# Optimization experiments

Measured on AMD Instinct MI355X. Metric: run time of the kernel, lower is better.

## Reference

```python
import jax, jax.numpy as jnp
import numpy as np

PC_MIN = jnp.array([0.0, -40.0, -3.0], dtype=jnp.float32)
VS_TOP = jnp.array([0.4, 0.4, 4.0], dtype=jnp.float32)
VS_MED = jnp.array([0.2, 0.2, 2.0], dtype=jnp.float32)
VS_LOW = jnp.array([0.1, 0.1, 1.0], dtype=jnp.float32)
GRID_TOP = (176, 200, 1)
GRID_MED = (352, 400, 2)
GRID_LOW = (704, 800, 4)
EPS = 1e-3
FILL = np.iinfo(np.int32).max


def _bn(x, g, b):
    # training-mode BatchNorm1d over the point/voxel axis (naiveSyncBN1d, eps=1e-3)
    mu = jnp.mean(x, axis=0)
    var = jnp.var(x, axis=0)
    return (x - mu) * jax.lax.rsqrt(var + EPS) * g + b


def _decode(lin, gx, gy, gz):
    x = lin % gx
    r = lin // gx
    y = r % gy
    r = r // gy
    z = r % gz
    b = r // gz
    return b, x, y, z


def _vfe(pts, batch, vs, grid, W1, g1, b1, W2, g2, b2):
    # Dynamic voxelization + DynamicScatterVFE (cluster center + voxel center, 2 layers, scatter-mean).
    N = pts.shape[0]
    gx, gy, gz = grid
    xyz = pts[:, :3]
    coors = jnp.floor((xyz - PC_MIN) / vs).astype(jnp.int32)
    cx = jnp.clip(coors[:, 0], 0, gx - 1)
    cy = jnp.clip(coors[:, 1], 0, gy - 1)
    cz = jnp.clip(coors[:, 2], 0, gz - 1)
    lin = ((batch * gz + cz) * gy + cy) * gx + cx  # linear voxel id incl. batch
    uniq, inv = jnp.unique(lin, return_inverse=True, size=N, fill_value=FILL)
    valid = uniq != FILL
    cnt = jnp.maximum(jax.ops.segment_sum(jnp.ones((N,), pts.dtype), inv, num_segments=N), 1.0)
    seg_mean = lambda v: jax.ops.segment_sum(v, inv, num_segments=N) / cnt[:, None]
    f_cluster = xyz - seg_mean(xyz)[inv]                      # offset from per-voxel point mean
    centers = PC_MIN + (jnp.stack([cx, cy, cz], axis=1).astype(pts.dtype) + 0.5) * vs
    f_center = xyz - centers                                   # offset from voxel center
    feats = jnp.concatenate([pts, f_cluster, f_center], axis=1)  # [N, 10]
    h = jax.nn.relu(_bn(feats @ W1, g1, b1))
    h = jnp.concatenate([h, seg_mean(h)[inv]], axis=1)           # point feat || gathered voxel feat
    h = jax.nn.relu(_bn(h @ W2, g2, b2))
    vox = seg_mean(h)
    return jnp.where(valid[:, None], vox, 0.0), uniq, valid


def _merge(sub_feats, sub_uniq, sub_valid, top_uniq, sub_grid, factor):
    # find_coordinate_indices + scatter_v2(mode='avg'): mean of child voxel feats per parent voxel.
    b, x, y, z = _decode(sub_uniq, *sub_grid)
    gx, gy, gz = GRID_TOP
    parent = ((b * gz + z // factor) * gy + y // factor) * gx + x // factor
    M = top_uniq.shape[0]
    pos = jnp.clip(jnp.searchsorted(top_uniq, parent), 0, M - 1)
    found = sub_valid & (top_uniq[pos] == parent)
    seg = jnp.where(found, pos, M)  # unmatched/padding rows dropped into slot M
    s = jax.ops.segment_sum(sub_feats, seg, num_segments=M + 1)[:M]
    c = jax.ops.segment_sum(found.astype(sub_feats.dtype), seg, num_segments=M + 1)[:M]
    return s / jnp.maximum(c, 1.0)[:, None]


def setup_inputs() -> dict:
    key = jax.random.key(0)
    ks = jax.random.split(key, 12)
    N, B = 262144, 2
    x = jax.random.uniform(ks[0], (N, 1), jnp.float32, 0.0, 70.4)
    y = jax.random.uniform(ks[1], (N, 1), jnp.float32, -40.0, 40.0)
    z = jax.random.uniform(ks[2], (N, 1), jnp.float32, -3.0, 1.0)
    inten = jax.random.uniform(ks[3], (N, 1), jnp.float32)
    bcol = jnp.repeat(jnp.arange(B, dtype=jnp.float32), N // B)[:, None]
    points = jnp.concatenate([bcol, x, y, z, inten], axis=1)
    lin_w = lambda k, i, o: jax.random.normal(k, (i, o), jnp.float32) * (1.0 / np.sqrt(i))
    return dict(
        points=points, batch_size=2,
        W1_top=lin_w(ks[4], 10, 64), g1_top=jnp.ones(64), b1_top=jnp.zeros(64),
        W2_top=lin_w(ks[5], 128, 128), g2_top=jnp.ones(128), b2_top=jnp.zeros(128),
        W1_med=lin_w(ks[6], 10, 32), g1_med=jnp.ones(32), b1_med=jnp.zeros(32),
        W2_med=lin_w(ks[7], 64, 64), g2_med=jnp.ones(64), b2_med=jnp.zeros(64),
        W1_low=lin_w(ks[8], 10, 32), g1_low=jnp.ones(32), b1_low=jnp.zeros(32),
        W2_low=lin_w(ks[9], 64, 64), g2_low=jnp.ones(64), b2_low=jnp.zeros(64),
    )


def reference(points, batch_size, W1_top, g1_top, b1_top, W2_top, g2_top, b2_top,
              W1_med, g1_med, b1_med, W2_med, g2_med, b2_med,
              W1_low, g1_low, b1_low, W2_low, g2_low, b2_low):
    batch = points[:, 0].astype(jnp.int32)
    pts = points[:, 1:]
    vf, top_uniq, top_valid = _vfe(pts, batch, VS_TOP, GRID_TOP, W1_top, g1_top, b1_top, W2_top, g2_top, b2_top)
    mfeat, med_uniq, med_valid = _vfe(pts, batch, VS_MED, GRID_MED, W1_med, g1_med, b1_med, W2_med, g2_med, b2_med)
    lfeat, low_uniq, low_valid = _vfe(pts, batch, VS_LOW, GRID_LOW, W1_low, g1_low, b1_low, W2_low, g2_low, b2_low)
    med_mean = _merge(mfeat, med_uniq, med_valid, top_uniq, GRID_MED, 2)
    low_mean = _merge(lfeat, low_uniq, low_valid, top_uniq, GRID_LOW, 4)
    merged = jnp.where(top_valid[:, None], jnp.concatenate([med_mean, low_mean], axis=1), 0.0)
    b, x, y, z = _decode(top_uniq, *GRID_TOP)
    coors = jnp.where(top_valid[:, None], jnp.stack([b, z, y, x], axis=1), -1)
    return vf, merged, coors
```

## Files before the change

### kernel.cpp

```cpp
#include <hip/hip_runtime.h>
#include <cstdint>
#include <cstddef>

#define NPTS 262144
#define BLK 256
#define TGX 176
#define TGY 200
#define TGZ 1

#define G_TOPC 70400
#define G_MEDC 1126400
#define G_LOWC 4505600

#define SCAN_ITEMS 32
#define SCAN_CHUNK (BLK*SCAN_ITEMS)
#define NB_T 9
#define NB_M 138
#define NB_L 550
#define BO_T 0
#define BO_M 16
#define BO_L 160
#define NBVT (G_TOPC/BLK)
#define NBVM (NPTS/BLK)
#define NBVL (NPTS/BLK)

#define Y2B2 (NPTS/64)
#define ST1BLKS 256
#define NHT 4400
#define NHM 8192
#define NJT 8800
#define NJM 16384
#define NCL 275

typedef __attribute__((ext_vector_type(8))) short bf16x8;
typedef __attribute__((ext_vector_type(4))) float f32x4;

struct SP {
  const float4* srt; const int* jr; const float4* vm;
  const float* W1; const float* W2;
  const float* g1; const float* b1; const float* g2; const float* b2;
  const int* cnt; const int* uniq; const int* woff; const int* U;
  float* segt; float* part1; float* part2;
  float* coef1; float* coef2;
  unsigned short* Y2;
  float* hout;
  int C1; int segstride; int gx, gy, gz; float vx, vy, vz;
};

__device__ __forceinline__ unsigned short f2bf(float v) {
  unsigned u = __float_as_uint(v);
  u += 0x7FFFu + ((u >> 16) & 1u);
  return (unsigned short)(u >> 16);
}
__device__ __forceinline__ float bf2f(unsigned short h) {
  return __uint_as_float((unsigned)h << 16);
}

__device__ __forceinline__ void pcoords(float x, float y, float z,
    float vx, float vy, float vz, int gx, int gy, int gz,
    int& cx, int& cy, int& cz) {
  cx = (int)floorf((x - 0.0f)  / vx);
  cy = (int)floorf((y + 40.0f) / vy);
  cz = (int)floorf((z + 3.0f)  / vz);
  cx = min(max(cx, 0), gx - 1);
  cy = min(max(cy, 0), gy - 1);
  cz = min(max(cz, 0), gz - 1);
}

__device__ __forceinline__ int lin3(float b, float x, float y, float z,
    float vx, float vy, float vz, int gx, int gy, int gz) {
  int cx, cy, cz; pcoords(x, y, z, vx, vy, vz, gx, gy, gz, cx, cy, cz);
  return (((int)b * gz + cz) * gy + cy) * gx + cx;
}

__device__ __forceinline__ void build_f(float4 p, float4 vm,
    float vx, float vy, float vz, int gx, int gy, int gz, float* f) {
  int cx, cy, cz; pcoords(p.x, p.y, p.z, vx, vy, vz, gx, gy, gz, cx, cy, cz);
  f[0] = p.x; f[1] = p.y; f[2] = p.z; f[3] = p.w;
  f[4] = p.x - vm.x;
  f[5] = p.y - vm.y;
  f[6] = p.z - vm.z;
  f[7] = p.x - (0.0f   + (cx + 0.5f)*vx);
  f[8] = p.y - (-40.0f + (cy + 0.5f)*vy);
  f[9] = p.z - (-3.0f  + (cz + 0.5f)*vz);
}

__global__ __launch_bounds__(BLK) void k_count3(const float* __restrict__ pts,
    int* __restrict__ ct, int* __restrict__ cm, int* __restrict__ cl) {
  int i = blockIdx.x * BLK + threadIdx.x;
  if (i >= NPTS) return;
  float b = pts[i*5+0], x = pts[i*5+1], y = pts[i*5+2], z = pts[i*5+3];
  atomicAdd(&ct[lin3(b,x,y,z, 0.4f,0.4f,4.0f, 176,200,1)], 1);
  atomicAdd(&cm[lin3(b,x,y,z, 0.2f,0.2f,2.0f, 352,400,2)], 1);
  atomicAdd(&cl[lin3(b,x,y,z, 0.1f,0.1f,1.0f, 704,800,4)], 1);
}

__global__ __launch_bounds__(BLK) void k_scan1_all(const int* __restrict__ ct,
    const int* __restrict__ cm, const int* __restrict__ cl,
    int2* __restrict__ bsum) {
  int bid = blockIdx.x;
  const int* cnt; int G, bo, cb;
  if (bid < NB_T)            { cnt = ct; G = G_TOPC; bo = BO_T; cb = bid; }
  else if (bid < NB_T+NB_M)  { cnt = cm; G = G_MEDC; bo = BO_M; cb = bid - NB_T; }
  else                       { cnt = cl; G = G_LOWC; bo = BO_L; cb = bid - NB_T - NB_M; }
  int base = cb * SCAN_CHUNK + threadIdx.x * SCAN_ITEMS;
  int so = 0, sp = 0;
  #pragma unroll
  for (int k = 0; k < SCAN_ITEMS; k++) {
    int j = base + k;
    if (j < G) { int c = cnt[j]; if (c > 0) { so++; sp += c; } }
  }
  __shared__ int sho[BLK], shp[BLK];
  sho[threadIdx.x] = so; shp[threadIdx.x] = sp; __syncthreads();
  for (int off = BLK/2; off > 0; off >>= 1) {
    if (threadIdx.x < off) {
      sho[threadIdx.x] += sho[threadIdx.x + off];
      shp[threadIdx.x] += shp[threadIdx.x + off];
    }
    __syncthreads();
  }
  if (threadIdx.x == 0) { int2 v; v.x = sho[0]; v.y = shp[0]; bsum[bo + cb] = v; }
}

__device__ void scan_pass(int2* bsum, int off, int nb, int* U,
                          int* so, int* sp) {
  int t = threadIdx.x;
  int vo = 0, vp = 0;
  if (t < nb) { int2 v = bsum[off + t]; vo = v.x; vp = v.y; }
  so[t] = vo; sp[t] = vp; __syncthreads();
  for (int o = 1; o < 1024; o <<= 1) {
    int ao = (t >= o) ? so[t - o] : 0;
    int ap = (t >= o) ? sp[t - o] : 0;
    __syncthreads();
    so[t] += ao; sp[t] += ap;
    __syncthreads();
  }
  if (t < nb) { int2 e; e.x = so[t] - vo; e.y = sp[t] - vp; bsum[off + t] = e; }
  if (t == 0) *U = so[1023];
  __syncthreads();
}

__global__ __launch_bounds__(1024) void k_scan2_all(int2* __restrict__ bsum,
    int* __restrict__ Ut, int* __restrict__ Um, int* __restrict__ Ul) {
  __shared__ int so[1024], sp[1024];
  scan_pass(bsum, BO_T, NB_T, Ut, so, sp);
  scan_pass(bsum, BO_M, NB_M, Um, so, sp);
  scan_pass(bsum, BO_L, NB_L, Ul, so, sp);
}

__global__ __launch_bounds__(BLK) void k_scan3_all(const int* __restrict__ ct,
    const int* __restrict__ cm, const int* __restrict__ cl,
    const int2* __restrict__ bsum,
    int* __restrict__ rkt, int* __restrict__ rkm, int* __restrict__ rkl,
    int* __restrict__ uqt, int* __restrict__ uqm, int* __restrict__ uql,
    int* __restrict__ wot, int* __restrict__ wom, int* __restrict__ wol) {
  int bid = blockIdx.x;
  const int* cnt; int G, bo, cb; int *rank, *uniq, *woff;
  if (bid < NB_T)           { cnt=ct; G=G_TOPC; bo=BO_T; cb=bid;            rank=rkt; uniq=uqt; woff=wot; }
  else if (bid < NB_T+NB_M) { cnt=cm; G=G_MEDC; bo=BO_M; cb=bid-NB_T;       rank=rkm; uniq=uqm; woff=wom; }
  else                      { cnt=cl; G=G_LOWC; bo=BO_L; cb=bid-NB_T-NB_M;  rank=rkl; uniq=uql; woff=wol; }
  int base = cb * SCAN_CHUNK + threadIdx.x * SCAN_ITEMS;
  int so = 0, sp = 0;
  #pragma unroll
  for (int k = 0; k < SCAN_ITEMS; k++) {
    int j = base + k;
    if (j < G) { int c = cnt[j]; if (c > 0) { so++; sp += c; } }
  }
  __shared__ int sho[BLK], shp[BLK];
  sho[threadIdx.x] = so; shp[threadIdx.x] = sp; __syncthreads();
  for (int off = 1; off < BLK; off <<= 1) {
    int ao = (threadIdx.x >= off) ? sho[threadIdx.x - off] : 0;
    int ap = (threadIdx.x >= off) ? shp[threadIdx.x - off] : 0;
    __syncthreads();
    sho[threadIdx.x] += ao; shp[threadIdx.x] += ap;
    __syncthreads();
  }
  int2 bb = bsum[bo + cb];
  int ro = bb.x + sho[threadIdx.x] - so;
  int po = bb.y + shp[threadIdx.x] - sp;
  for (int k = 0; k < SCAN_ITEMS; k++) {
    int j = base + k;
    if (j < G) {
      int c = cnt[j];
      if (c > 0) { rank[j] = ro; uniq[ro] = j; woff[ro] = po; ro++; po += c; }
    }
  }
}

__global__ __launch_bounds__(BLK) void k_scatter3(const float* __restrict__ pts,
    const int* __restrict__ rkt, int* __restrict__ wot, float4* __restrict__ st, int* __restrict__ jt,
    const int* __restrict__ rkm, int* __restrict__ wom, float4* __restrict__ sm, int* __restrict__ jm,
    const int* __restrict__ rkl, int* __restrict__ wol, float4* __restrict__ sl, int* __restrict__ jl) {
  int i = blockIdx.x * BLK + threadIdx.x;
  if (i >= NPTS) return;
  float b = pts[i*5+0], x = pts[i*5+1], y = pts[i*5+2], z = pts[i*5+3], it = pts[i*5+4];
  float4 p; p.x = x; p.y = y; p.z = z; p.w = it;
  {
    int r = rkt[lin3(b,x,y,z, 0.4f,0.4f,4.0f, 176,200,1)];
    int j = atomicAdd(&wot[r], 1); st[j] = p; jt[j] = r;
  }
  {
    int r = rkm[lin3(b,x,y,z, 0.2f,0.2f,2.0f, 352,400,2)];
    int j = atomicAdd(&wom[r], 1); sm[j] = p; jm[j] = r;
  }
  {
    int r = rkl[lin3(b,x,y,z, 0.1f,0.1f,1.0f, 704,800,4)];
    int j = atomicAdd(&wol[r], 1); sl[j] = p; jl[j] = r;
  }
}

__global__ __launch_bounds__(BLK) void k_vox13(
    const float4* __restrict__ st, const int* __restrict__ uqt, const int* __restrict__ ct,
    const int* __restrict__ wot, const int* __restrict__ Ut, float4* __restrict__ vt,
    const float4* __restrict__ sm, const int* __restrict__ uqm, const int* __restrict__ cm,
    const int* __restrict__ wom, const int* __restrict__ Um, float4* __restrict__ vm,
    const float4* __restrict__ sl, const int* __restrict__ uql, const int* __restrict__ cl,
    const int* __restrict__ wol, const int* __restrict__ Ul, float4* __restrict__ vl) {
  int bid = blockIdx.x;
  const float4* srt; const int *uniq, *cnt, *woff, *Up; float4* vmean; int r;
  if (bid < NBVT)           { r = bid*BLK + threadIdx.x;           srt=st; uniq=uqt; cnt=ct; woff=wot; Up=Ut; vmean=vt; }
  else if (bid < NBVT+NBVM) { r = (bid-NBVT)*BLK + threadIdx.x;    srt=sm; uniq=uqm; cnt=cm; woff=wom; Up=Um; vmean=vm; }
  else                      { r = (bid-NBVT-NBVM)*BLK + threadIdx.x; srt=sl; uniq=uql; cnt=cl; woff=wol; Up=Ul; vmean=vl; }
  if (r >= *Up) return;
  int lin = uniq[r];
  int len = cnt[lin];
  int base = woff[r] - len;
  float sx = 0.f, sy = 0.f, sz = 0.f;
  for (int k = 0; k < len; k++) {
    float4 p = srt[base + k];
    sx += p.x; sy += p.y; sz += p.z;
  }
  float il = 1.0f / (float)len;
  float4 o; o.x = sx*il; o.y = sy*il; o.z = sz*il; o.w = il;
  vmean[r] = o;
}

__global__ __launch_bounds__(BLK) void k_stats1_all(SP a, SP b, SP c) {
  int s = blockIdx.x >> 8;
  int blk = blockIdx.x & 255;
  SP sp = (s == 0) ? a : ((s == 1) ? b : c);
  const int C1 = sp.C1;
  __shared__ float w[640];
  __shared__ float wsum[4][64], wsq[4][64];
  for (int t = threadIdx.x; t < 10*C1; t += BLK) w[t] = sp.W1[t];
  __syncthreads();
  float f[4][10];
  #pragma unroll
  for (int k = 0; k < 4; k++) {
    int i = blk*1024 + k*BLK + threadIdx.x;
    float4 p = sp.srt[i];
    float4 vmn = sp.vm[sp.jr[i]];
    build_f(p, vmn, sp.vx, sp.vy, sp.vz, sp.gx, sp.gy, sp.gz, f[k]);
  }
  int wv = threadIdx.x >> 6;
  int lane = threadIdx.x & 63;
  for (int o = 0; o < C1; o += 4) {
    float sacc[4] = {0,0,0,0}, qacc[4] = {0,0,0,0};
    #pragma unroll
    for (int k = 0; k < 4; k++) {
      float a0=0.f, a1=0.f, a2=0.f, a3=0.f;
      #pragma unroll
      for (int d = 0; d < 10; d++) {
        float fv = f[k][d];
        const float* wr = &w[d*C1 + o];
        a0 = fmaf(fv, wr[0], a0); a1 = fmaf(fv, wr[1], a1);
        a2 = fmaf(fv, wr[2], a2); a3 = fmaf(fv, wr[3], a3);
      }
      sacc[0] += a0; sacc[1] += a1; sacc[2] += a2; sacc[3] += a3;
      qacc[0] += a0*a0; qacc[1] += a1*a1; qacc[2] += a2*a2; qacc[3] += a3*a3;
    }
    #pragma unroll
    for (int m = 1; m < 64; m <<= 1) {
      #pragma unroll
      for (int e = 0; e < 4; e++) {
        sacc[e] += __shfl_xor(sacc[e], m);
        qacc[e] += __shfl_xor(qacc[e], m);
      }
    }
    if (lane == 0) {
      #pragma unroll
      for (int e = 0; e < 4; e++) { wsum[wv][o+e] = sacc[e]; wsq[wv][o+e] = qacc[e]; }
    }
  }
  __syncthreads();
  if (threadIdx.x < C1) {
    int ch = threadIdx.x;
    float sv = wsum[0][ch] + wsum[1][ch] + wsum[2][ch] + wsum[3][ch];
    float qv = wsq[0][ch] + wsq[1][ch] + wsq[2][ch] + wsq[3][ch];
    sp.part1[(size_t)blk*2*C1 + ch]      = sv;
    sp.part1[(size_t)blk*2*C1 + C1 + ch] = qv;
  }
}

__device__ __forceinline__ void partcoef_body(const float* part, int NB, int C,
    int ch, const float* g, const float* b, float* coef) {
  float s = 0.f, q = 0.f;
  for (int bk = threadIdx.x; bk < NB; bk += BLK) {
    s += part[(size_t)bk*2*C + ch];
    q += part[(size_t)bk*2*C + C + ch];
  }
  __shared__ float ss[BLK], sq[BLK];
  ss[threadIdx.x] = s; sq[threadIdx.x] = q; __syncthreads();
  for (int off = BLK/2; off > 0; off >>= 1) {
    if (threadIdx.x < off) {
      ss[threadIdx.x] += ss[threadIdx.x + off];
      sq[threadIdx.x] += sq[threadIdx.x + off];
    }
    __syncthreads();
  }
  if (threadIdx.x == 0) {
    float mu  = ss[0] * (1.0f / NPTS);
    float var = sq[0] * (1.0f / NPTS) - mu*mu;
    float sc  = g[ch] * (1.0f / sqrtf(var + 1e-3f));
    coef[ch]     = sc;
    coef[C + ch] = fmaf(-mu, sc, b[ch]);
  }
}

__global__ __launch_bounds__(BLK) void k_partcoef1_all(SP a, SP b, SP c) {
  int bid = blockIdx.x; SP sp; int ch;
  if (bid < 64)      { sp = a; ch = bid; }
  else if (bid < 96) { sp = b; ch = bid - 64; }
  else               { sp = c; ch = bid - 96; }
  if (ch >= sp.C1) return;
  partcoef_body(sp.part1, ST1BLKS, sp.C1, ch, sp.g1, sp.b1, sp.coef1);
}

__global__ __launch_bounds__(BLK) void k_partcoef2_all(SP a, SP b, SP c) {
  int bid = blockIdx.x; SP sp; int ch;
  if (bid < 128)      { sp = a; ch = bid; }
  else if (bid < 192) { sp = b; ch = bid - 128; }
  else                { sp = c; ch = bid - 192; }
  if (ch >= 2*sp.C1) return;
  partcoef_body(sp.part2, Y2B2, 2*sp.C1, ch, sp.g2, sp.b2, sp.coef2);
}

__global__ __launch_bounds__(BLK) void k_hsegT_all(SP a, SP b, SP c) {
  int bid = blockIdx.x; SP sp; int rb;
  if (bid < NHT)           { sp = a; rb = bid; }
  else if (bid < NHT+NHM)  { sp = b; rb = bid - NHT; }
  else                     { sp = c; rb = bid - NHT - NHM; }
  const int C1 = sp.C1;
  const int qsh = (C1 == 64) ? 4 : 3;
  __shared__ float w[640];
  __shared__ float sc[64], sb[64];
  for (int t = threadIdx.x; t < 10*C1; t += BLK) w[t] = sp.W1[t];
  for (int t = threadIdx.x; t < C1; t += BLK) { sc[t] = sp.coef1[t]; sb[t] = sp.coef1[C1 + t]; }
  __syncthreads();
  int tid = rb * BLK + threadIdx.x;
  int r = tid >> qsh;
  int q = tid & ((1 << qsh) - 1);
  if (r >= *sp.U) return;
  int lin = sp.uniq[r];
  int len = sp.cnt[lin];
  int base = sp.woff[r] - len;
  float4 vmn = sp.vm[r];
  int c0 = q * 4;
  float s0 = sc[c0+0], s1 = sc[c0+1], s2 = sc[c0+2], s3 = sc[c0+3];
  float o0 = sb[c0+0], o1 = sb[c0+1], o2 = sb[c0+2], o3 = sb[c0+3];
  float a0=0.f, a1=0.f, a2=0.f, a3=0.f;
  for (int k = 0; k < len; k++) {
    float4 p = sp.srt[base + k];
    float f[10];
    build_f(p, vmn, sp.vx, sp.vy, sp.vz, sp.gx, sp.gy, sp.gz, f);
    float y0=0.f, y1=0.f, y2=0.f, y3=0.f;
    #pragma unroll
    for (int d = 0; d < 10; d++) {
      float fv = f[d];
      const float* wr = &w[d*C1 + c0];
      y0 = fmaf(fv, wr[0], y0); y1 = fmaf(fv, wr[1], y1);
      y2 = fmaf(fv, wr[2], y2); y3 = fmaf(fv, wr[3], y3);
    }
    a0 += fmaxf(fmaf(y0, s0, o0), 0.f);
    a1 += fmaxf(fmaf(y1, s1, o1), 0.f);
    a2 += fmaxf(fmaf(y2, s2, o2), 0.f);
    a3 += fmaxf(fmaf(y3, s3, o3), 0.f);
  }
  float il = 1.0f / (float)len;
  sp.segt[(size_t)(c0+0)*sp.segstride + r] = a0*il;
  sp.segt[(size_t)(c0+1)*sp.segstride + r] = a1*il;
  sp.segt[(size_t)(c0+2)*sp.segstride + r] = a2*il;
  sp.segt[(size_t)(c0+3)*sp.segstride + r] = a3*il;
}

__global__ __launch_bounds__(BLK) void k_packB_all(
    const float* __restrict__ W2t_, unsigned short* __restrict__ Bt,
    const float* __restrict__ W2m_, unsigned short* __restrict__ Bm,
    const float* __restrict__ W2l_, unsigned short* __restrict__ Bl) {
  int bid = blockIdx.x;
  const float* W2; unsigned short* Bp; int C2, idx;
  if (bid < 64)      { W2 = W2t_; Bp = Bt; C2 = 128; idx = bid*BLK + threadIdx.x; }
  else if (bid < 80) { W2 = W2m_; Bp = Bm; C2 = 64;  idx = (bid-64)*BLK + threadIdx.x; }
  else               { W2 = W2l_; Bp = Bl; C2 = 64;  idx = (bid-80)*BLK + threadIdx.x; }
  if (idx >= C2*C2) return;
  int NCF = C2/16;
  int per_kb = NCF*512;
  int kb = idx / per_kb, rem = idx % per_kb;
  int cf = rem / 512, r2 = rem % 512;
  int lane = r2 >> 3, j = r2 & 7;
  int k = kb*32 + (lane >> 4)*8 + j;
  int col = cf*16 + (lane & 15);
  Bp[idx] = f2bf(W2[(size_t)k*C2 + col]);
}

template<int C1>
__device__ __forceinline__ void y2m_body(const SP& sp,
    const unsigned short* __restrict__ Bpk, int blk, unsigned short* Alds) {
  constexpr int K   = 2*C1;
  constexpr int C2  = 2*C1;
  constexpr int MT  = 64;
  constexpr int NKB = K / 32;
  constexpr int NCF = C2 / 16;
  constexpr int RB  = K * 2;
  const int tid  = threadIdx.x;
  const int base = blk * MT;

  {
    const int jst = tid & 63;
    const int qst = tid >> 6;
    int jr = sp.jr[base + jst];
    float4 p = sp.srt[base + jst];
    float4 vmn = sp.vm[jr];
    float fs[10];
    build_f(p, vmn, sp.vx, sp.vy, sp.vz, sp.gx, sp.gy, sp.gz, fs);
    const int k_lo = qst * (K/4);
    #pragma unroll
    for (int kk = 0; kk < K/8; kk++) {
      int k0 = k_lo + kk*2;
      float v0, v1;
      if (k0 < C1) {
        float y0 = 0.f, y1v = 0.f;
        #pragma unroll
        for (int d = 0; d < 10; d++) {
          y0  = fmaf(fs[d], sp.W1[d*C1 + k0],     y0);
          y1v = fmaf(fs[d], sp.W1[d*C1 + k0 + 1], y1v);
        }
        v0 = fmaxf(fmaf(y0,  sp.coef1[k0],   sp.coef1[C1 + k0]),   0.f);
        v1 = fmaxf(fmaf(y1v, sp.coef1[k0+1], sp.coef1[C1 + k0+1]), 0.f);
      } else {
        v0 = sp.segt[(size_t)(k0     - C1)*sp.segstride + jr];
        v1 = sp.segt[(size_t)(k0 + 1 - C1)*sp.segstride + jr];
      }
      unsigned u = (unsigned)f2bf(v0) | ((unsigned)f2bf(v1) << 16);
      int g  = k0 >> 3;
      int gp = g ^ (jst & 7);
      *(unsigned*)((char*)Alds + (size_t)jst*RB + gp*16 + (k0 & 7)*2) = u;
    }
  }
  __syncthreads();

  const int w    = tid >> 6;
  const int l    = tid & 63;
  const int rowf = l & 15;
  const int kg   = l >> 4;
  const int row  = w*16 + rowf;
  f32x4 acc[NCF];
  #pragma unroll
  for (int cf = 0; cf < NCF; cf++) acc[cf] = (f32x4){0.f, 0.f, 0.f, 0.f};
  #pragma unroll
  for (int kb = 0; kb < NKB; kb++) {
    int g  = kb*4 + kg;
    int gp = g ^ (row & 7);
    bf16x8 a = *(const bf16x8*)((const char*)Alds + (size_t)row*RB + gp*16);
    const bf16x8* bfr = (const bf16x8*)Bpk + (size_t)(kb*NCF)*64 + l;
    #pragma unroll
    for (int cf = 0; cf < NCF; cf++) {
      bf16x8 b = bfr[cf*64];
      acc[cf] = __builtin_amdgcn_mfma_f32_16x16x32_bf16(a, b, acc[cf], 0, 0, 0);
    }
  }

  __syncthreads();
  float* red = (float*)Alds;
  #pragma unroll
  for (int cf = 0; cf < NCF; cf++) {
    f32x4 v = acc[cf];
    float sv = v.x + v.y + v.z + v.w;
    float qv = v.x*v.x + v.y*v.y + v.z*v.z + v.w*v.w;
    red[(w*4 + kg)*C2 + cf*16 + rowf]        = sv;
    red[(16 + w*4 + kg)*C2 + cf*16 + rowf]   = qv;
  }
  __syncthreads();
  if (tid < C2) {
    float sv = 0.f, qv = 0.f;
    #pragma unroll 4
    for (int i = 0; i < 16; i++) {
      sv += red[i*C2 + tid];
      qv += red[(16 + i)*C2 + tid];
    }
    sp.part2[(size_t)blk*2*C2 + tid]      = sv;
    sp.part2[(size_t)blk*2*C2 + C2 + tid] = qv;
  }
  __syncthreads();

  unsigned short* D = Alds;
  #pragma unroll
  for (int cf = 0; cf < NCF; cf++) {
    #pragma unroll
    for (int rg = 0; rg < 4; rg++) {
      int rr = w*16 + kg*4 + rg;
      D[rr*C2 + cf*16 + rowf] = f2bf(acc[cf][rg]);
    }
  }
  __syncthreads();
  for (int it = tid; it < MT*C2/8; it += BLK) {
    int r = (it*8) / C2;
    int c = (it*8) % C2;
    uint4 v = *(const uint4*)&D[it*8];
    *(uint4*)&sp.Y2[(size_t)(base + r)*C2 + c] = v;
  }
}

__global__ __launch_bounds__(BLK) void k_y2m_all(SP a, SP b, SP c,
    const unsigned short* __restrict__ Bt, const unsigned short* __restrict__ Bm,
    const unsigned short* __restrict__ Bl) {
  __shared__ unsigned short Alds[64*128];
  int bid = blockIdx.x;
  if (bid < Y2B2)        y2m_body<64>(a, Bt, bid, Alds);
  else if (bid < 2*Y2B2) y2m_body<32>(b, Bm, bid - Y2B2, Alds);
  else                   y2m_body<32>(c, Bl, bid - 2*Y2B2, Alds);
}

__global__ __launch_bounds__(BLK) void k_hseg2_all(SP a, SP b, SP c) {
  int bid = blockIdx.x; SP sp; int rb;
  if (bid < NJT)           { sp = a; rb = bid; }
  else if (bid < NJT+NJM)  { sp = b; rb = bid - NJT; }
  else                     { sp = c; rb = bid - NJT - NJM; }
  const int C = 2*sp.C1;
  const int qsh = (C == 128) ? 5 : 4;
  __shared__ float sc[128], sb[128];
  for (int t = threadIdx.x; t < C; t += BLK) { sc[t] = sp.coef2[t]; sb[t] = sp.coef2[C + t]; }
  __syncthreads();
  int tid = rb * BLK + threadIdx.x;
  int r = tid >> qsh;
  int q = tid & ((1 << qsh) - 1);
  if (r >= *sp.U) return;
  int lin = sp.uniq[r];
  int len = sp.cnt[lin];
  int base = sp.woff[r] - len;
  int c0 = q * 4;
  float s0 = sc[c0+0], s1 = sc[c0+1], s2 = sc[c0+2], s3 = sc[c0+3];
  float o0 = sb[c0+0], o1 = sb[c0+1], o2 = sb[c0+2], o3 = sb[c0+3];
  float a0=0.f, a1=0.f, a2=0.f, a3=0.f;
  const unsigned short* Yh = sp.Y2;
  for (int k = 0; k < len; k++) {
    ushort4 hv = *(const ushort4*)&Yh[(size_t)(base + k)*C + c0];
    a0 += fmaxf(fmaf(bf2f(hv.x), s0, o0), 0.f);
    a1 += fmaxf(fmaf(bf2f(hv.y), s1, o1), 0.f);
    a2 += fmaxf(fmaf(bf2f(hv.z), s2, o2), 0.f);
    a3 += fmaxf(fmaf(bf2f(hv.w), s3, o3), 0.f);
  }
  float il = 1.0f / (float)len;
  float4 o = {a0*il, a1*il, a2*il, a3*il};
  *(float4*)&sp.hout[(size_t)r*C + c0] = o;
}

__global__ __launch_bounds__(BLK) void k_clist_all(const int* __restrict__ tuniq,
    const int* __restrict__ Utp,
    const int* __restrict__ cnt_m, const int* __restrict__ rank_m,
    int* __restrict__ clist_m, int* __restrict__ mcnt_m,
    const int* __restrict__ cnt_l, const int* __restrict__ rank_l,
    int* __restrict__ clist_l, int* __restrict__ mcnt_l) {
  int bid = blockIdx.x;
  const int *scnt, *srank; int *clist, *mcnt;
  int gx, gy, gz, f, rb;
  if (bid < NCL) { scnt=cnt_m; srank=rank_m; clist=clist_m; mcnt=mcnt_m;
                   gx=352; gy=400; gz=2; f=2; rb=bid; }
  else           { scnt=cnt_l; srank=rank_l; clist=clist_l; mcnt=mcnt_l;
                   gx=704; gy=800; gz=4; f=4; rb=bid-NCL; }
  int r = rb * BLK + threadIdx.x;
  if (r >= *Utp) return;
  int lin = tuniq[r];
  int x = lin % TGX; int t = lin / TGX;
  int y = t % TGY;   int b = t / TGY;
  int m = 0;
  for (int cz = 0; cz < gz; cz++)
    for (int yy = y*f; yy < y*f + f; yy++)
      for (int xx = x*f; xx < x*f + f; xx++) {
        int cl = ((b*gz + cz)*gy + yy)*gx + xx;
        if (scnt[cl] > 0) clist[(size_t)r*64 + (m++)] = srank[cl];
      }
  mcnt[r] = m;
}

__global__ __launch_bounds__(BLK) void k_merge2_all(
    const float* __restrict__ vox_m, const int* __restrict__ clist_m,
    const int* __restrict__ mcnt_m, float* __restrict__ maccm,
    const float* __restrict__ vox_l, const int* __restrict__ clist_l,
    const int* __restrict__ mcnt_l, float* __restrict__ maccl,
    const int* __restrict__ Utp) {
  int bid = blockIdx.x;
  const float* vox; const int *clist, *mcnt; float* dest; int rb;
  if (bid < NHT) { vox=vox_m; clist=clist_m; mcnt=mcnt_m; dest=maccm; rb=bid; }
  else           { vox=vox_l; clist=clist_l; mcnt=mcnt_l; dest=maccl; rb=bid-NHT; }
  int idx = rb * BLK + threadIdx.x;
  int r = idx >> 4;
  int q = idx & 15;
  if (r >= *Utp) return;
  int m = mcnt[r];
  float a0=0.f, a1=0.f, a2=0.f, a3=0.f;
  for (int t = 0; t < m; t++) {
    int cr = clist[(size_t)r*64 + t];
    float4 v = *(const float4*)&vox[(size_t)cr*64 + q*4];
    a0 += v.x; a1 += v.y; a2 += v.z; a3 += v.w;
  }
  float inv = 1.0f / (float)max(m, 1);
  float4 o = {a0*inv, a1*inv, a2*inv, a3*inv};
  *(float4*)&dest[(size_t)r*64 + q*4] = o;
}

__global__ __launch_bounds__(BLK) void k_fin_all(const int* __restrict__ uniq,
    const int* __restrict__ Up, const float* __restrict__ maccm,
    const float* __restrict__ maccl, float* __restrict__ vf,
    float* __restrict__ mg, float* __restrict__ coors) {
  int idx = blockIdx.x * BLK + threadIdx.x;
  int r = idx >> 5;
  int q = idx & 31;
  if (r >= NPTS) return;
  int U = *Up;
  float4 v = {0.f, 0.f, 0.f, 0.f};
  if (r < U)
    v = (q < 16) ? *(const float4*)&maccm[(size_t)r*64 + q*4]
                 : *(const float4*)&maccl[(size_t)r*64 + (q-16)*4];
  *(float4*)&mg[(size_t)r*128 + q*4] = v;
  if (r >= U) {
    float4 z = {0.f, 0.f, 0.f, 0.f};
    *(float4*)&vf[(size_t)r*128 + q*4] = z;
  }
  if (q == 0) {
    float4 co;
    if (r < U) {
      int lin = uniq[r];
      int x = lin % TGX; int t = lin / TGX;
      int y = t % TGY;   t /= TGY;
      int z = t % TGZ;   int b = t / TGZ;
      co.x = (float)b; co.y = (float)z; co.z = (float)y; co.w = (float)x;
    } else {
      co.x = -1.f; co.y = -1.f; co.z = -1.f; co.w = -1.f;
    }
    *(float4*)&coors[(size_t)r*4] = co;
  }
}

extern "C" void kernel_launch(void* const* d_in, const int* in_sizes, int n_in,
                              void* d_out, int out_size, void* d_ws, size_t ws_size,
                              hipStream_t stream) {
  const float* pts = (const float*)d_in[0];

  float* out = (float*)d_out;
  float* vf = out;
  float* mg = out + (size_t)NPTS * 128;
  float* co = out + (size_t)NPTS * 256;

  char* w = (char*)d_ws;
  size_t off = 0;
  auto alloc = [&](size_t bytes) -> void* {
    void* p = w + off;
    off = (off + bytes + 1023) & ~(size_t)1023;
    return p;
  };
  int*    cnt_t   = (int*)alloc(((size_t)G_TOPC + G_MEDC + G_LOWC) * 4);
  int*    cnt_m   = cnt_t + G_TOPC;
  int*    cnt_l   = cnt_t + G_TOPC + G_MEDC;
  int*    rank_t  = (int*)alloc((size_t)G_TOPC * 4);
  int*    rank_m  = (int*)alloc((size_t)G_MEDC * 4);
  int*    rank_l  = (int*)alloc((size_t)G_LOWC * 4);
  int*    uniq_t  = (int*)alloc((size_t)G_TOPC * 4);
  int*    uniq_m  = (int*)alloc((size_t)NPTS * 4);
  int*    uniq_l  = (int*)alloc((size_t)NPTS * 4);
  int*    woff_t  = (int*)alloc((size_t)G_TOPC * 4);
  int*    woff_m  = (int*)alloc((size_t)NPTS * 4);
  int*    woff_l  = (int*)alloc((size_t)NPTS * 4);
  float4* srt_t   = (float4*)alloc((size_t)NPTS * 16);
  float4* srt_m   = (float4*)alloc((size_t)NPTS * 16);
  float4* srt_l   = (float4*)alloc((size_t)NPTS * 16);
  int*    jr_t    = (int*)alloc((size_t)NPTS * 4);
  int*    jr_m    = (int*)alloc((size_t)NPTS * 4);
  int*    jr_l    = (int*)alloc((size_t)NPTS * 4);
  float4* vm_t    = (float4*)alloc((size_t)G_TOPC * 16);
  float4* vm_m    = (float4*)alloc((size_t)NPTS * 16);
  float4* vm_l    = (float4*)alloc((size_t)NPTS * 16);
  float*  segt_t  = (float*)alloc((size_t)G_TOPC * 64 * 4);
  float*  segt_m  = (float*)alloc((size_t)NPTS * 32 * 4);
  float*  segt_l  = (float*)alloc((size_t)NPTS * 32 * 4);
  float*  vox_m   = (float*)alloc((size_t)NPTS * 64 * 4);
  float*  vox_l   = (float*)alloc((size_t)NPTS * 64 * 4);
  unsigned short* Y2h_t = (unsigned short*)alloc((size_t)NPTS * 128 * 2);
  unsigned short* Y2h_m = (unsigned short*)alloc((size_t)NPTS * 64 * 2);
  unsigned short* Y2h_l = (unsigned short*)alloc((size_t)NPTS * 64 * 2);
  unsigned short* Bpk_t = (unsigned short*)alloc(16384 * 2);
  unsigned short* Bpk_m = (unsigned short*)alloc(4096 * 2);
  unsigned short* Bpk_l = (unsigned short*)alloc(4096 * 2);
  int*    clist_m = (int*)alloc((size_t)G_TOPC * 64 * 4);
  int*    clist_l = (int*)alloc((size_t)G_TOPC * 64 * 4);
  int*    mcnt_m  = (int*)alloc((size_t)G_TOPC * 4);
  int*    mcnt_l  = (int*)alloc((size_t)G_TOPC * 4);
  float*  maccm   = (float*)alloc((size_t)G_TOPC * 64 * 4);
  float*  maccl   = (float*)alloc((size_t)G_TOPC * 64 * 4);
  float*  part1_t = (float*)alloc((size_t)ST1BLKS * 128 * 4);
  float*  part1_m = (float*)alloc((size_t)ST1BLKS * 64 * 4);
  float*  part1_l = (float*)alloc((size_t)ST1BLKS * 64 * 4);
  float*  part2_t = (float*)alloc((size_t)Y2B2 * 256 * 4);
  float*  part2_m = (float*)alloc((size_t)Y2B2 * 128 * 4);
  float*  part2_l = (float*)alloc((size_t)Y2B2 * 128 * 4);
  float*  coef    = (float*)alloc(6 * 256 * 4);
  int2*   bsum    = (int2*)alloc(1024 * 8);
  int*    Ut      = (int*)alloc(64);
  int*    Um      = (int*)alloc(64);
  int*    Ul      = (int*)alloc(64);
  (void)in_sizes; (void)n_in; (void)out_size; (void)ws_size;

  auto mkSP = [&](int scaleIdx) -> SP {
    SP s{};
    if (scaleIdx == 0) {
      s.srt = srt_t; s.jr = jr_t; s.vm = vm_t;
      s.W1 = (const float*)d_in[2];  s.g1 = (const float*)d_in[3];
      s.b1 = (const float*)d_in[4];  s.W2 = (const float*)d_in[5];
      s.g2 = (const float*)d_in[6];  s.b2 = (const float*)d_in[7];
      s.cnt = cnt_t; s.uniq = uniq_t; s.woff = woff_t; s.U = Ut;
      s.segt = segt_t; s.part1 = part1_t; s.part2 = part2_t;
      s.coef1 = coef + 0*256; s.coef2 = coef + 1*256;
      s.Y2 = Y2h_t; s.hout = vf;
      s.C1 = 64; s.segstride = G_TOPC;
      s.gx = 176; s.gy = 200; s.gz = 1; s.vx = 0.4f; s.vy = 0.4f; s.vz = 4.0f;
    } else if (scaleIdx == 1) {
      s.srt = srt_m; s.jr = jr_m; s.vm = vm_m;
      s.W1 = (const float*)d_in[8];  s.g1 = (const float*)d_in[9];
      s.b1 = (const float*)d_in[10]; s.W2 = (const float*)d_in[11];
      s.g2 = (const float*)d_in[12]; s.b2 = (const float*)d_in[13];
      s.cnt = cnt_m; s.uniq = uniq_m; s.woff = woff_m; s.U = Um;
      s.segt = segt_m; s.part1 = part1_m; s.part2 = part2_m;
      s.coef1 = coef + 2*256; s.coef2 = coef + 3*256;
      s.Y2 = Y2h_m; s.hout = vox_m;
      s.C1 = 32; s.segstride = NPTS;
      s.gx = 352; s.gy = 400; s.gz = 2; s.vx = 0.2f; s.vy = 0.2f; s.vz = 2.0f;
    } else {
      s.srt = srt_l; s.jr = jr_l; s.vm = vm_l;
      s.W1 = (const float*)d_in[14]; s.g1 = (const float*)d_in[15];
      s.b1 = (const float*)d_in[16]; s.W2 = (const float*)d_in[17];
      s.g2 = (const float*)d_in[18]; s.b2 = (const float*)d_in[19];
      s.cnt = cnt_l; s.uniq = uniq_l; s.woff = woff_l; s.U = Ul;
      s.segt = segt_l; s.part1 = part1_l; s.part2 = part2_l;
      s.coef1 = coef + 4*256; s.coef2 = coef + 5*256;
      s.Y2 = Y2h_l; s.hout = vox_l;
      s.C1 = 32; s.segstride = NPTS;
      s.gx = 704; s.gy = 800; s.gz = 4; s.vx = 0.1f; s.vy = 0.1f; s.vz = 1.0f;
    }
    return s;
  };
  SP spT = mkSP(0), spM = mkSP(1), spL = mkSP(2);

  k_packB_all<<<96, BLK, 0, stream>>>((const float*)d_in[5], Bpk_t,
      (const float*)d_in[11], Bpk_m, (const float*)d_in[17], Bpk_l);

  (void)hipMemsetAsync(cnt_t, 0, ((size_t)G_TOPC + G_MEDC + G_LOWC) * 4, stream);
  k_count3<<<NPTS/BLK, BLK, 0, stream>>>(pts, cnt_t, cnt_m, cnt_l);
  k_scan1_all<<<NB_T + NB_M + NB_L, BLK, 0, stream>>>(cnt_t, cnt_m, cnt_l, bsum);
  k_scan2_all<<<1, 1024, 0, stream>>>(bsum, Ut, Um, Ul);
  k_scan3_all<<<NB_T + NB_M + NB_L, BLK, 0, stream>>>(cnt_t, cnt_m, cnt_l, bsum,
      rank_t, rank_m, rank_l, uniq_t, uniq_m, uniq_l, woff_t, woff_m, woff_l);
  k_clist_all<<<2*NCL, BLK, 0, stream>>>(uniq_t, Ut,
      cnt_m, rank_m, clist_m, mcnt_m, cnt_l, rank_l, clist_l, mcnt_l);
  k_scatter3<<<NPTS/BLK, BLK, 0, stream>>>(pts,
      rank_t, woff_t, srt_t, jr_t,
      rank_m, woff_m, srt_m, jr_m,
      rank_l, woff_l, srt_l, jr_l);
  k_vox13<<<NBVT + NBVM + NBVL, BLK, 0, stream>>>(
      srt_t, uniq_t, cnt_t, woff_t, Ut, vm_t,
      srt_m, uniq_m, cnt_m, woff_m, Um, vm_m,
      srt_l, uniq_l, cnt_l, woff_l, Ul, vm_l);

  k_stats1_all<<<3*ST1BLKS, BLK, 0, stream>>>(spT, spM, spL);
  k_partcoef1_all<<<128, BLK, 0, stream>>>(spT, spM, spL);
  k_hsegT_all<<<NHT + 2*NHM, BLK, 0, stream>>>(spT, spM, spL);
  k_y2m_all<<<3*Y2B2, BLK, 0, stream>>>(spT, spM, spL, Bpk_t, Bpk_m, Bpk_l);
  k_partcoef2_all<<<256, BLK, 0, stream>>>(spT, spM, spL);
  k_hseg2_all<<<NJT + 2*NJM, BLK, 0, stream>>>(spT, spM, spL);

  k_merge2_all<<<2*NHT, BLK, 0, stream>>>(vox_m, clist_m, mcnt_m, maccm,
      vox_l, clist_l, mcnt_l, maccl, Ut);
  k_fin_all<<<(NPTS*32)/BLK, BLK, 0, stream>>>(uniq_t, Ut, maccm, maccl,
      vf, mg, co);
}
```

Baseline: 692.1 us.

## Compute BN1 stats from feature moments and write merge output directly into final buffer

The first BatchNorm's mean and variance are now derived from the first and second moments of the 10-dim input features (10 sums plus 55 cross-products) instead of computing all C1 projected channels per point. A tiny 3-block kernel reduces the moments and projects them through W1 to produce the scale and shift coefficients, replacing the per-channel partcoef kernel. The merge kernel also writes straight into the output merged buffer, removing the intermediate maccm/maccl arrays and the copy in the final kernel. Risks include 65 live registers per thread with a 65-wide shuffle reduction, and E[y^2]-mu^2 is more prone to precision loss.

```diff
diff --git a/kernel.cpp b/kernel.cpp
--- a/kernel.cpp
+++ b/kernel.cpp
@@ -235,60 +235,84 @@
   vmean[r] = o;
 }
 
-__global__ __launch_bounds__(BLK) void k_stats1_all(SP a, SP b, SP c) {
+__global__ __launch_bounds__(BLK) void k_fmom_all(SP a, SP b, SP c) {
   int s = blockIdx.x >> 8;
   int blk = blockIdx.x & 255;
   SP sp = (s == 0) ? a : ((s == 1) ? b : c);
-  const int C1 = sp.C1;
-  __shared__ float w[640];
-  __shared__ float wsum[4][64], wsq[4][64];
-  for (int t = threadIdx.x; t < 10*C1; t += BLK) w[t] = sp.W1[t];
-  __syncthreads();
-  float f[4][10];
+  float m[65];
+  #pragma unroll
+  for (int i = 0; i < 65; i++) m[i] = 0.f;
   #pragma unroll
   for (int k = 0; k < 4; k++) {
     int i = blk*1024 + k*BLK + threadIdx.x;
     float4 p = sp.srt[i];
     float4 vmn = sp.vm[sp.jr[i]];
-    build_f(p, vmn, sp.vx, sp.vy, sp.vz, sp.gx, sp.gy, sp.gz, f[k]);
-  }
+    float f[10];
+    build_f(p, vmn, sp.vx, sp.vy, sp.vz, sp.gx, sp.gy, sp.gz, f);
+    int idx = 10;
+    #pragma unroll
+    for (int d = 0; d < 10; d++) {
+      m[d] += f[d];
+      #pragma unroll
+      for (int e = d; e < 10; e++) {
+        m[idx] = fmaf(f[d], f[e], m[idx]);
+        idx++;
+      }
+    }
+  }
+  #pragma unroll
+  for (int st = 1; st < 64; st <<= 1) {
+    #pragma unroll
+    for (int i = 0; i < 65; i++) m[i] += __shfl_xor(m[i], st);
+  }
+  __shared__ float ws[4][65];
   int wv = threadIdx.x >> 6;
   int lane = threadIdx.x & 63;
-  for (int o = 0; o < C1; o += 4) {
-    float sacc[4] = {0,0,0,0}, qacc[4] = {0,0,0,0};
-    #pragma unroll
-    for (int k = 0; k < 4; k++) {
-      float a0=0.f, a1=0.f, a2=0.f, a3=0.f;
+  if (lane == 0) {
+    #pragma unroll
+    for (int i = 0; i < 65; i++) ws[wv][i] = m[i];
+  }
+  __syncthreads();
+  if (threadIdx.x < 65) {
+    int t = threadIdx.x;
+    sp.part1[(size_t)blk*65 + t] = ws[0][t] + ws[1][t] + ws[2][t] + ws[3][t];
+  }
+}
+
+__global__ __launch_bounds__(BLK) void k_mcoef_all(SP a, SP b, SP c) {
+  SP sp = (blockIdx.x == 0) ? a : ((blockIdx.x == 1) ? b : c);
+  const int C1 = sp.C1;
+  __shared__ float M[65];
+  int t = threadIdx.x;
+  if (t < 65) {
+    float s = 0.f;
+    #pragma unroll 8
+    for (int bk = 0; bk < ST1BLKS; bk++) s += sp.part1[(size_t)bk*65 + t];
+    M[t] = s * (1.0f / NPTS);
+  }
+  __syncthreads();
+  if (t < C1) {
+    float wv[10];
+    #pragma unroll
+    for (int d = 0; d < 10; d++) wv[d] = sp.W1[d*C1 + t];
+    float mu = 0.f;
+    #pragma unroll
+    for (int d = 0; d < 10; d++) mu = fmaf(M[d], wv[d], mu);
+    float ey2 = 0.f;
+    int idx = 10;
+    #pragma unroll
+    for (int d = 0; d < 10; d++) {
       #pragma unroll
-      for (int d = 0; d < 10; d++) {
-        float fv = f[k][d];
-        const float* wr = &w[d*C1 + o];
-        a0 = fmaf(fv, wr[0], a0); a1 = fmaf(fv, wr[1], a1);
-        a2 = fmaf(fv, wr[2], a2); a3 = fmaf(fv, wr[3], a3);
+      for (int e = d; e < 10; e++) {
+        float c2 = M[idx] * wv[d] * wv[e];
+        ey2 += (e == d) ? c2 : 2.0f * c2;
+        idx++;
       }
-      sacc[0] += a0; sacc[1] += a1; sacc[2] += a2; sacc[3] += a3;
-      qacc[0] += a0*a0; qacc[1] += a1*a1; qacc[2] += a2*a2; qacc[3] += a3*a3;
-    }
-    #pragma unroll
-    for (int m = 1; m < 64; m <<= 1) {
-      #pragma unroll
-      for (int e = 0; e < 4; e++) {
-        sacc[e] += __shfl_xor(sacc[e], m);
-        qacc[e] += __shfl_xor(qacc[e], m);
-      }
-    }
-    if (lane == 0) {
-      #pragma unroll
-      for (int e = 0; e < 4; e++) { wsum[wv][o+e] = sacc[e]; wsq[wv][o+e] = qacc[e]; }
-    }
-  }
-  __syncthreads();
-  if (threadIdx.x < C1) {
-    int ch = threadIdx.x;
-    float sv = wsum[0][ch] + wsum[1][ch] + wsum[2][ch] + wsum[3][ch];
-    float qv = wsq[0][ch] + wsq[1][ch] + wsq[2][ch] + wsq[3][ch];
-    sp.part1[(size_t)blk*2*C1 + ch]      = sv;
-    sp.part1[(size_t)blk*2*C1 + C1 + ch] = qv;
+    }
+    float var = ey2 - mu*mu;
+    float sc  = sp.g1[t] * (1.0f / sqrtf(var + 1e-3f));
+    sp.coef1[t]      = sc;
+    sp.coef1[C1 + t] = fmaf(-mu, sc, sp.b1[t]);
   }
 }
 
@@ -315,15 +339,6 @@
     coef[ch]     = sc;
     coef[C + ch] = fmaf(-mu, sc, b[ch]);
   }
-}
-
-__global__ __launch_bounds__(BLK) void k_partcoef1_all(SP a, SP b, SP c) {
-  int bid = blockIdx.x; SP sp; int ch;
-  if (bid < 64)      { sp = a; ch = bid; }
-  else if (bid < 96) { sp = b; ch = bid - 64; }
-  else               { sp = c; ch = bid - 96; }
-  if (ch >= sp.C1) return;
-  partcoef_body(sp.part1, ST1BLKS, sp.C1, ch, sp.g1, sp.b1, sp.coef1);
 }
 
 __global__ __launch_bounds__(BLK) void k_partcoef2_all(SP a, SP b, SP c) {
@@ -585,14 +600,14 @@
 
 __global__ __launch_bounds__(BLK) void k_merge2_all(
     const float* __restrict__ vox_m, const int* __restrict__ clist_m,
-    const int* __restrict__ mcnt_m, float* __restrict__ maccm,
+    const int* __restrict__ mcnt_m,
     const float* __restrict__ vox_l, const int* __restrict__ clist_l,
-    const int* __restrict__ mcnt_l, float* __restrict__ maccl,
-    const int* __restrict__ Utp) {
+    const int* __restrict__ mcnt_l,
+    const int* __restrict__ Utp, float* __restrict__ mg) {
   int bid = blockIdx.x;
-  const float* vox; const int *clist, *mcnt; float* dest; int rb;
-  if (bid < NHT) { vox=vox_m; clist=clist_m; mcnt=mcnt_m; dest=maccm; rb=bid; }
-  else           { vox=vox_l; clist=clist_l; mcnt=mcnt_l; dest=maccl; rb=bid-NHT; }
+  const float* vox; const int *clist, *mcnt; int half, rb;
+  if (bid < NHT) { vox=vox_m; clist=clist_m; mcnt=mcnt_m; half=0; rb=bid; }
+  else           { vox=vox_l; clist=clist_l; mcnt=mcnt_l; half=64; rb=bid-NHT; }
   int idx = rb * BLK + threadIdx.x;
   int r = idx >> 4;
   int q = idx & 15;
@@ -606,25 +621,20 @@
   }
   float inv = 1.0f / (float)max(m, 1);
   float4 o = {a0*inv, a1*inv, a2*inv, a3*inv};
-  *(float4*)&dest[(size_t)r*64 + q*4] = o;
+  *(float4*)&mg[(size_t)r*128 + half + q*4] = o;
 }
 
 __global__ __launch_bounds__(BLK) void k_fin_all(const int* __restrict__ uniq,
-    const int* __restrict__ Up, const float* __restrict__ maccm,
-    const float* __restrict__ maccl, float* __restrict__ vf,
+    const int* __restrict__ Up, float* __restrict__ vf,
     float* __restrict__ mg, float* __restrict__ coors) {
   int idx = blockIdx.x * BLK + threadIdx.x;
   int r = idx >> 5;
   int q = idx & 31;
   if (r >= NPTS) return;
   int U = *Up;
-  float4 v = {0.f, 0.f, 0.f, 0.f};
-  if (r < U)
-    v = (q < 16) ? *(const float4*)&maccm[(size_t)r*64 + q*4]
-                 : *(const float4*)&maccl[(size_t)r*64 + (q-16)*4];
-  *(float4*)&mg[(size_t)r*128 + q*4] = v;
   if (r >= U) {
     float4 z = {0.f, 0.f, 0.f, 0.f};
+    *(float4*)&mg[(size_t)r*128 + q*4] = z;
     *(float4*)&vf[(size_t)r*128 + q*4] = z;
   }
   if (q == 0) {
@@ -695,11 +705,9 @@
   int*    clist_l = (int*)alloc((size_t)G_TOPC * 64 * 4);
   int*    mcnt_m  = (int*)alloc((size_t)G_TOPC * 4);
   int*    mcnt_l  = (int*)alloc((size_t)G_TOPC * 4);
-  float*  maccm   = (float*)alloc((size_t)G_TOPC * 64 * 4);
-  float*  maccl   = (float*)alloc((size_t)G_TOPC * 64 * 4);
   float*  part1_t = (float*)alloc((size_t)ST1BLKS * 128 * 4);
-  float*  part1_m = (float*)alloc((size_t)ST1BLKS * 64 * 4);
-  float*  part1_l = (float*)alloc((size_t)ST1BLKS * 64 * 4);
+  float*  part1_m = (float*)alloc((size_t)ST1BLKS * 128 * 4);
+  float*  part1_l = (float*)alloc((size_t)ST1BLKS * 128 * 4);
   float*  part2_t = (float*)alloc((size_t)Y2B2 * 256 * 4);
   float*  part2_m = (float*)alloc((size_t)Y2B2 * 128 * 4);
   float*  part2_l = (float*)alloc((size_t)Y2B2 * 128 * 4);
@@ -770,15 +778,14 @@
       srt_m, uniq_m, cnt_m, woff_m, Um, vm_m,
       srt_l, uniq_l, cnt_l, woff_l, Ul, vm_l);
 
-  k_stats1_all<<<3*ST1BLKS, BLK, 0, stream>>>(spT, spM, spL);
-  k_partcoef1_all<<<128, BLK, 0, stream>>>(spT, spM, spL);
+  k_fmom_all<<<3*ST1BLKS, BLK, 0, stream>>>(spT, spM, spL);
+  k_mcoef_all<<<3, BLK, 0, stream>>>(spT, spM, spL);
   k_hsegT_all<<<NHT + 2*NHM, BLK, 0, stream>>>(spT, spM, spL);
   k_y2m_all<<<3*Y2B2, BLK, 0, stream>>>(spT, spM, spL, Bpk_t, Bpk_m, Bpk_l);
   k_partcoef2_all<<<256, BLK, 0, stream>>>(spT, spM, spL);
   k_hseg2_all<<<NJT + 2*NJM, BLK, 0, stream>>>(spT, spM, spL);
 
-  k_merge2_all<<<2*NHT, BLK, 0, stream>>>(vox_m, clist_m, mcnt_m, maccm,
-      vox_l, clist_l, mcnt_l, maccl, Ut);
-  k_fin_all<<<(NPTS*32)/BLK, BLK, 0, stream>>>(uniq_t, Ut, maccm, maccl,
-      vf, mg, co);
-}
+  k_merge2_all<<<2*NHT, BLK, 0, stream>>>(vox_m, clist_m, mcnt_m,
+      vox_l, clist_l, mcnt_l, Ut, mg);
+  k_fin_all<<<(NPTS*32)/BLK, BLK, 0, stream>>>(uniq_t, Ut, vf, mg, co);
+}
```

Result: no change. 683.7 us (-1.2%).
